# Performance work log

Measured on AMD Instinct MI355X. Metric: run time of the kernel, lower is better.

Reference implementation:

```python
import jax, jax.numpy as jnp
import numpy as np

N_HEAD = 16
SPARSE_TOPK = 64
NEG_INF = float('-inf')


def setup_inputs() -> dict:
    key = jax.random.key(0)
    ks = jax.random.split(key, 12)
    B, T, C = 4, 1024, 1024
    s = 0.02
    q = jax.random.normal(ks[0], (B, T, C), jnp.float32)
    kv = jax.random.normal(ks[1], (B, T, C), jnp.float32)  # forward asserts k == v
    tgt_mask = jnp.tril(jnp.ones((T, T), jnp.bool_)).reshape(1, 1, T, T)
    inp = {'q': q, 'k': kv, 'v': kv, 'tgt_mask': tgt_mask}
    for i, n in enumerate(['Wq', 'Wk', 'Wv', 'Wo']):
        inp[n] = jax.random.normal(ks[2 + i], (C, C), jnp.float32) * s
    for i, n in enumerate(['bq', 'bk', 'bv', 'bo']):
        inp[n] = jax.random.normal(ks[6 + i], (C,), jnp.float32) * s
    return inp


def reference(q, k, v, tgt_mask, Wq, Wk, Wv, Wo, bq, bk, bv, bo):
    B, T, C = q.shape
    H = N_HEAD
    hd = C // H
    scale = 1.0 / np.sqrt(hd).astype(np.float32)
    # QKV projections -> [B, H, T, hd]
    qh = (q @ Wq + bq).reshape(B, T, H, hd).transpose(0, 2, 1, 3)
    kh = (k @ Wk + bk).reshape(B, T, H, hd).transpose(0, 2, 1, 3)
    vh = (v @ Wv + bv).reshape(B, T, H, hd).transpose(0, 2, 1, 3)
    # full attention scores [B, H, T, T]
    att = jnp.einsum('bhtd,bhsd->bhts', qh, kh) * scale
    # causal mask: masked_fill where tgt_mask == 0
    att = jnp.where(tgt_mask[:, :, :T, :T], att, NEG_INF)
    # top-k sparse pruning: keep entries >= k-th largest per row (ties kept)
    top, _ = jax.lax.top_k(att, SPARSE_TOPK)
    vk = top[..., -1:]  # [B, H, T, 1]
    att = jnp.where(att < vk, NEG_INF, att)
    att = jax.nn.softmax(att, axis=-1)
    # dropout is identity in eval (p=0.0)
    y = jnp.einsum('bhts,bhsd->bhtd', att, vh)
    y = y.transpose(0, 2, 1, 3).reshape(B, T, C)
    return y @ Wo + bo
```

## Files before the change

kernel.cpp:

```cpp
#include <hip/hip_runtime.h>
#include <hip/hip_bf16.h>
#include <math.h>

typedef __attribute__((ext_vector_type(8))) short short8;
typedef __attribute__((ext_vector_type(4))) float f32x4;
typedef __attribute__((ext_vector_type(4))) int int4v;

#define SCL 0.1803368801111204f

static __device__ __forceinline__ unsigned short f2bf(float f) {
  unsigned u = __float_as_uint(f);
  u = u + 0x7FFFu + ((u >> 16) & 1u);
  return (unsigned short)(u >> 16);
}

static __device__ __forceinline__ unsigned keyof(float x) {
  unsigned u = __float_as_uint(x);
  return (u & 0x80000000u) ? ~u : (u | 0x80000000u);
}
static __device__ __forceinline__ float keyinv(unsigned k) {
  unsigned u = (k & 0x80000000u) ? (k & 0x7FFFFFFFu) : ~k;
  return __uint_as_float(u);
}

static __device__ __forceinline__ int saddr(int r, int cc) {
  return (((r << 9) + cc) << 2) ^ ((r & 7) << 4);
}
static __device__ __forceinline__ int paddr(int r, int c) {
  return ((r << 11) + (c << 1)) ^ ((r & 7) << 4);
}

static __device__ __forceinline__ void gld_lds16(const unsigned short* g, unsigned short* l) {
  __builtin_amdgcn_global_load_lds(
      (const __attribute__((address_space(1))) void*)g,
      (__attribute__((address_space(3))) void*)l, 16, 0, 0);
}

__global__ __launch_bounds__(256) void cvt3_k(const float* __restrict__ q,
                                              const float* __restrict__ k,
                                              const float* __restrict__ v,
                                              unsigned short* __restrict__ oq,
                                              unsigned short* __restrict__ ok,
                                              unsigned short* __restrict__ ov) {
  const int y = blockIdx.y;
  const float* in = (y == 0) ? q : (y == 1) ? k : v;
  unsigned short* out = (y == 0) ? oq : (y == 1) ? ok : ov;
  const int i = blockIdx.x * 256 + threadIdx.x;
  const f32x4* p = (const f32x4*)in + 2 * (size_t)i;
  f32x4 a = p[0], b = p[1];
  short8 r;
  r[0] = (short)f2bf(a[0]); r[1] = (short)f2bf(a[1]);
  r[2] = (short)f2bf(a[2]); r[3] = (short)f2bf(a[3]);
  r[4] = (short)f2bf(b[0]); r[5] = (short)f2bf(b[1]);
  r[6] = (short)f2bf(b[2]); r[7] = (short)f2bf(b[3]);
  ((short8*)out)[i] = r;
}

__global__ __launch_bounds__(256) void wtrans4_k(const float* __restrict__ Wq,
                                                 const float* __restrict__ Wk,
                                                 const float* __restrict__ Wv,
                                                 const float* __restrict__ Wo,
                                                 unsigned short* __restrict__ Wqt,
                                                 unsigned short* __restrict__ Wkt,
                                                 unsigned short* __restrict__ Wvt,
                                                 unsigned short* __restrict__ Wot) {
  const int z = blockIdx.z;
  const float* W = (z == 0) ? Wq : (z == 1) ? Wk : (z == 2) ? Wv : Wo;
  unsigned short* Wt = (z == 0) ? Wqt : (z == 1) ? Wkt : (z == 2) ? Wvt : Wot;
  __shared__ float tile[32][33];
  const int tx = threadIdx.x, ty = threadIdx.y;
  const int x0 = blockIdx.x * 32, y0 = blockIdx.y * 32;
#pragma unroll
  for (int j = 0; j < 4; ++j)
    tile[ty + j * 8][tx] = W[(y0 + ty + j * 8) * 1024 + x0 + tx];
  __syncthreads();
#pragma unroll
  for (int j = 0; j < 4; ++j)
    Wt[(x0 + ty + j * 8) * 1024 + (y0 + tx)] = f2bf(tile[tx][ty + j * 8]);
}

template <int MODE>
static __device__ __forceinline__ void gemm_body(unsigned short* As, unsigned short* Bs,
                                                 const unsigned short* __restrict__ A,
                                                 const unsigned short* __restrict__ Bt,
                                                 const float* __restrict__ bias,
                                                 void* __restrict__ out) {
  const int tid = threadIdx.x;
  const int lane = tid & 63, w = tid >> 6;
  const int wr = w >> 1, wc = w & 1;
  const int m0 = blockIdx.y * 128, n0 = blockIdx.x * 128;
  const int l15 = lane & 15, l4 = lane >> 4;
  f32x4 acc[4][4] = {};
  const int r0 = tid >> 2, s0 = (tid & 3) * 8;
  const int r1 = r0 + 64;
  const unsigned short* gA0 = A + (m0 + r0) * 1024 + s0;
  const unsigned short* gA1 = A + (m0 + r1) * 1024 + s0;
  const unsigned short* gB0 = Bt + (n0 + r0) * 1024 + s0;
  const unsigned short* gB1 = Bt + (n0 + r1) * 1024 + s0;
  unsigned short* lA0 = As + r0 * 32 + s0;
  unsigned short* lA1 = As + r1 * 32 + s0;
  unsigned short* lB0 = Bs + r0 * 32 + s0;
  unsigned short* lB1 = Bs + r1 * 32 + s0;

  for (int kt = 0; kt < 32; ++kt) {
    const int k0 = kt * 32;
    __syncthreads();
    gld_lds16(gA0 + k0, lA0);
    gld_lds16(gA1 + k0, lA1);
    gld_lds16(gB0 + k0, lB0);
    gld_lds16(gB1 + k0, lB1);
    __syncthreads();
    short8 af[4], bfr[4];
#pragma unroll
    for (int i = 0; i < 4; ++i) {
      af[i]  = *(const short8*)(As + (wr * 64 + i * 16 + l15) * 32 + l4 * 8);
      bfr[i] = *(const short8*)(Bs + (wc * 64 + i * 16 + l15) * 32 + l4 * 8);
    }
#pragma unroll
    for (int i = 0; i < 4; ++i)
#pragma unroll
      for (int j = 0; j < 4; ++j)
        acc[i][j] = __builtin_amdgcn_mfma_f32_16x16x32_bf16(af[i], bfr[j], acc[i][j], 0, 0, 0);
  }
#pragma unroll
  for (int i = 0; i < 4; ++i) {
#pragma unroll
    for (int j = 0; j < 4; ++j) {
      const int n = n0 + wc * 64 + j * 16 + l15;
      const float bv = bias[n];
#pragma unroll
      for (int r = 0; r < 4; ++r) {
        const int m = m0 + wr * 64 + i * 16 + l4 * 4 + r;
        const float v = acc[i][j][r] + bv;
        if (MODE == 2) {
          ((float*)out)[m * 1024 + n] = v;
        } else {
          const int bb = m >> 10, t = m & 1023, hh = n >> 6, dd = n & 63;
          const unsigned short bfv = f2bf(v);
          if (MODE == 0)
            ((unsigned short*)out)[(((bb << 4) + hh) * 1024 + t) * 64 + dd] = bfv;
          else
            ((unsigned short*)out)[(((bb << 4) + hh) * 64 + dd) * 1024 + t] = bfv;
        }
      }
    }
  }
}

__global__ __launch_bounds__(256) void gemm_qkv_k(
    const unsigned short* qbf, const unsigned short* kbf, const unsigned short* vbf,
    const unsigned short* Wqt, const unsigned short* Wkt, const unsigned short* Wvt,
    const float* bq, const float* bk, const float* bv,
    unsigned short* Qh, unsigned short* Kh, unsigned short* Vth) {
  __shared__ unsigned short As[128 * 32], Bs[128 * 32];
  const int z = blockIdx.z;
  const unsigned short* A  = (z == 0) ? qbf : ((z == 1) ? kbf : vbf);
  const unsigned short* Bt = (z == 0) ? Wqt : ((z == 1) ? Wkt : Wvt);
  const float* bias        = (z == 0) ? bq  : ((z == 1) ? bk  : bv);
  if (z == 2) gemm_body<1>(As, Bs, A, Bt, bias, Vth);
  else        gemm_body<0>(As, Bs, A, Bt, bias, z ? Kh : Qh);
}

__global__ __launch_bounds__(256) void gemm_out_k(const unsigned short* Y,
                                                  const unsigned short* Wot,
                                                  const float* bo, float* out) {
  __shared__ unsigned short As[128 * 32], Bs[128 * 32];
  gemm_body<2>(As, Bs, Y, Wot, bo, out);
}

__global__ __launch_bounds__(512, 6) void attn_k(const unsigned short* __restrict__ Q,
                                                 const unsigned short* __restrict__ K,
                                                 const unsigned short* __restrict__ Vt,
                                                 unsigned short* __restrict__ Y) {
  extern __shared__ __align__(16) char smem[];
  const int tid = threadIdx.x, lane = tid & 63, w = tid >> 6;
  const int t0 = (63 - blockIdx.x) * 16;
  const int h = blockIdx.y, b = blockIdx.z;
  const unsigned short* Qp = Q + (((b * 16 + h) * 1024) + t0) * 64;
  const unsigned short* Kh = K + (b * 16 + h) * 65536;
  const unsigned short* Vh = Vt + (b * 16 + h) * 65536;
  const int L = t0 + 16;
  const int Lpad = (L + 31) & ~31;
  const int nCT = L >> 4;
  const int l15 = lane & 15, l4 = lane >> 4;
  float* RED  = (float*)(smem + 32768);
  float* RED2 = (float*)(smem + 32768 + 4352);

  const short8 aq0 = *(const short8*)(Qp + l15 * 64 + l4 * 8);
  const short8 aq1 = *(const short8*)(Qp + l15 * 64 + 32 + l4 * 8);

  auto qk_chunk = [&](int tlo, int thi) {
    for (int ct = tlo + w; ct < thi; ct += 8) {
      const int c0 = ct * 16;
      const short8 kb0 = *(const short8*)(Kh + (c0 + l15) * 64 + l4 * 8);
      const short8 kb1 = *(const short8*)(Kh + (c0 + l15) * 64 + 32 + l4 * 8);
      f32x4 acc = {0.f, 0.f, 0.f, 0.f};
      acc = __builtin_amdgcn_mfma_f32_16x16x32_bf16(aq0, kb0, acc, 0, 0, 0);
      acc = __builtin_amdgcn_mfma_f32_16x16x32_bf16(aq1, kb1, acc, 0, 0, 0);
      const int c = c0 + l15, cc = c & 511;
      if (ct == nCT - 1) {
#pragma unroll
        for (int r = 0; r < 4; ++r) {
          const int row = l4 * 4 + r;
          *(float*)(smem + saddr(row, cc)) = (c <= t0 + row) ? acc[r] * SCL : -INFINITY;
        }
      } else {
#pragma unroll
        for (int r = 0; r < 4; ++r)
          *(float*)(smem + saddr(l4 * 4 + r, cc)) = acc[r] * SCL;
      }
    }
  };

  auto process_row = [&](float (&v)[16], int r, int Lr) {
    float lm = v[0];
#pragma unroll
    for (int i = 1; i < 16; ++i) lm = fmaxf(lm, v[i]);
    float mx = lm, mn = lm;
#pragma unroll
    for (int o = 32; o; o >>= 1) {
      mx = fmaxf(mx, __shfl_xor(mx, o));
      mn = fminf(mn, __shfl_xor(mn, o));
    }
    float thr = -INFINITY;
    if (Lr > 64) {
      unsigned lo = (unsigned)__builtin_amdgcn_readfirstlane((int)keyof(mn));
      unsigned hi = (unsigned)__builtin_amdgcn_readfirstlane((int)keyof(mx)) + 1u;
      int cl = Lr, ch = 0;
      int alt = 0;
      while (hi - lo > 1u) {
        const unsigned span = hi - lo;
        unsigned off;
        if (alt) off = span >> 1;
        else {
          const float fr = (float)(cl - 64) / (float)(cl - ch);
          off = (unsigned)(fr * (float)span);
          if (off < 1u) off = 1u;
          if (off > span - 1u) off = span - 1u;
        }
        alt ^= 1;
        const unsigned mid = lo + off;
        const float tm = keyinv(mid);
        int cnt = 0;
#pragma unroll
        for (int i = 0; i < 16; ++i) cnt += (int)__popcll(__ballot(v[i] >= tm));
        if (cnt >= 64) { lo = mid; cl = cnt; if (cnt == 64) break; }
        else { hi = mid; ch = cnt; }
      }
      thr = keyinv(lo);
    }
    float s = 0.f;
#pragma unroll
    for (int i = 0; i < 16; ++i) {
      const float pv = (v[i] >= thr) ? exp2f(v[i] - mx) : 0.f;
      v[i] = pv;
      s += pv;
    }
#pragma unroll
    for (int o = 32; o; o >>= 1) s += __shfl_xor(s, o);
    if (lane == 0) RED2[r] = 1.f / s;
#pragma unroll
    for (int p = 0; p < 8; ++p) {
      const int c = ((p & 3) << 7) + (lane << 1) + ((p >= 4) ? 512 : 0);
      if (c < Lpad) {
        const unsigned pk = (unsigned)f2bf(v[2 * p]) | ((unsigned)f2bf(v[2 * p + 1]) << 16);
        *(unsigned*)(smem + paddr(r, c)) = pk;
      }
    }
  };

  qk_chunk(0, (nCT < 32) ? nCT : 32);
  __syncthreads();

  const int rA = w * 2, rB = rA + 1;
  const int LrA = t0 + rA + 1, LrB = t0 + rB + 1;
  float vA[16], vB[16];
#pragma unroll
  for (int p = 0; p < 4; ++p) {
    const int c = (p << 7) + (lane << 1);
    const float2 tA = *(const float2*)(smem + saddr(rA, c));
    const float2 tB = *(const float2*)(smem + saddr(rB, c));
    const bool vld = c < L;
    vA[2 * p]     = vld ? tA.x : -INFINITY;
    vA[2 * p + 1] = vld ? tA.y : -INFINITY;
    vB[2 * p]     = vld ? tB.x : -INFINITY;
    vB[2 * p + 1] = vld ? tB.y : -INFINITY;
  }
  __syncthreads();
  if (L > 512) qk_chunk(32, nCT);
  __syncthreads();

#pragma unroll
  for (int p = 0; p < 4; ++p) {
    const int cc = (p << 7) + (lane << 1);
    const float2 tA = *(const float2*)(smem + saddr(rA, cc));
    const bool vld = (cc + 512) < L;
    vA[8 + 2 * p] = vld ? tA.x : -INFINITY;
    vA[9 + 2 * p] = vld ? tA.y : -INFINITY;
  }
  process_row(vA, rA, LrA);

#pragma unroll
  for (int p = 0; p < 4; ++p) {
    const int cc = (p << 7) + (lane << 1);
    const float2 tB = *(const float2*)(smem + saddr(rB, cc));
    const bool vld = (cc + 512) < L;
    vB[8 + 2 * p] = vld ? tB.x : -INFINITY;
    vB[9 + 2 * p] = vld ? tB.y : -INFINITY;
  }
  process_row(vB, rB, LrB);
  __syncthreads();

  const int nST = Lpad >> 5;
  const int stMid = (nST + 1) >> 1;
  const int d0 = (w & 3) * 16;
  const int stLo = (w < 4) ? 0 : stMid;
  const int stHi = (w < 4) ? stMid : nST;
  f32x4 acc = {0.f, 0.f, 0.f, 0.f};
  for (int st = stLo; st < stHi; ++st) {
    const int sb = st * 32 + l4 * 8;
    const short8 paf = *(const short8*)(smem + paddr(l15, sb));
    const short8 vb = *(const short8*)(Vh + (d0 + l15) * 1024 + sb);
    acc = __builtin_amdgcn_mfma_f32_16x16x32_bf16(paf, vb, acc, 0, 0, 0);
  }
  if (w >= 4) {
    const int base = (w - 4) * 272 + l15;
#pragma unroll
    for (int r = 0; r < 4; ++r) RED[base + (l4 * 4 + r) * 17] = acc[r];
  }
  __syncthreads();
  if (w < 4) {
    const int base = w * 272 + l15;
    const int d = (h << 6) + d0 + l15;
#pragma unroll
    for (int r = 0; r < 4; ++r) {
      const float inv = RED2[l4 * 4 + r];
      const float vr = (acc[r] + RED[base + (l4 * 4 + r) * 17]) * inv;
      const int tg = t0 + l4 * 4 + r;
      Y[((b << 10) + tg) * 1024 + d] = f2bf(vr);
    }
  }
}

extern "C" void kernel_launch(void* const* d_in, const int* in_sizes, int n_in,
                              void* d_out, int out_size, void* d_ws, size_t ws_size,
                              hipStream_t stream) {
  const float* q  = (const float*)d_in[0];
  const float* k  = (const float*)d_in[1];
  const float* v  = (const float*)d_in[2];
  const float* Wq = (const float*)d_in[4];
  const float* Wk = (const float*)d_in[5];
  const float* Wv = (const float*)d_in[6];
  const float* Wo = (const float*)d_in[7];
  const float* bq = (const float*)d_in[8];
  const float* bk = (const float*)d_in[9];
  const float* bv = (const float*)d_in[10];
  const float* bo = (const float*)d_in[11];

  char* ws = (char*)d_ws;
  const size_t MB = 1u << 20;
  unsigned short* qbf = (unsigned short*)(ws + 0 * MB);
  unsigned short* kbf = (unsigned short*)(ws + 8 * MB);
  unsigned short* vbf = (unsigned short*)(ws + 16 * MB);
  unsigned short* Wqt = (unsigned short*)(ws + 24 * MB);
  unsigned short* Wkt = (unsigned short*)(ws + 26 * MB);
  unsigned short* Wvt = (unsigned short*)(ws + 28 * MB);
  unsigned short* Wot = (unsigned short*)(ws + 30 * MB);
  unsigned short* Qh  = (unsigned short*)(ws + 32 * MB);
  unsigned short* Kh  = (unsigned short*)(ws + 40 * MB);
  unsigned short* Vth = (unsigned short*)(ws + 48 * MB);
  unsigned short* Y   = qbf;

  cvt3_k<<<dim3(2048, 3), 256, 0, stream>>>(q, k, v, qbf, kbf, vbf);
  wtrans4_k<<<dim3(32, 32, 4), dim3(32, 8), 0, stream>>>(Wq, Wk, Wv, Wo, Wqt, Wkt, Wvt, Wot);
  gemm_qkv_k<<<dim3(8, 32, 3), 256, 0, stream>>>(qbf, kbf, vbf, Wqt, Wkt, Wvt,
                                                 bq, bk, bv, Qh, Kh, Vth);
  attn_k<<<dim3(64, 16, 4), 512, 37248, stream>>>(Qh, Kh, Vth, Y);
  gemm_out_k<<<dim3(8, 32), 256, 0, stream>>>(Y, Wot, bo, (float*)d_out);
}
```

Measured before the change: 230.6 us.

## Halve attention LDS footprint by chunking scores and P into 256/512-column slices

The score buffer now holds 256 columns instead of 512, so QK^T is computed in four column chunks, each followed by a register gather. The bf16 P matrix is kept packed in registers and written to LDS in two 512-column halves, each consumed by its own PV MFMA pass. Shared memory per block drops from about 37KB to about 21KB, which should allow more resident blocks per CU. The cost is extra __syncthreads barriers and more live registers for the packed P values.

```diff
diff --git a/kernel.cpp b/kernel.cpp
--- a/kernel.cpp
+++ b/kernel.cpp
@@ -24,10 +24,10 @@
 }
 
 static __device__ __forceinline__ int saddr(int r, int cc) {
-  return (((r << 9) + cc) << 2) ^ ((r & 7) << 4);
-}
-static __device__ __forceinline__ int paddr(int r, int c) {
-  return ((r << 11) + (c << 1)) ^ ((r & 7) << 4);
+  return (((r << 8) + cc) << 2) ^ ((r & 7) << 4);
+}
+static __device__ __forceinline__ int paddr(int r, int lc) {
+  return ((r << 10) + (lc << 1)) ^ ((r & 7) << 4);
 }
 
 static __device__ __forceinline__ void gld_lds16(const unsigned short* g, unsigned short* l) {
@@ -183,8 +183,8 @@
   const int Lpad = (L + 31) & ~31;
   const int nCT = L >> 4;
   const int l15 = lane & 15, l4 = lane >> 4;
-  float* RED  = (float*)(smem + 32768);
-  float* RED2 = (float*)(smem + 32768 + 4352);
+  float* RED  = (float*)(smem + 16384);
+  float* RED2 = (float*)(smem + 16384 + 4352);
 
   const short8 aq0 = *(const short8*)(Qp + l15 * 64 + l4 * 8);
   const short8 aq1 = *(const short8*)(Qp + l15 * 64 + 32 + l4 * 8);
@@ -197,7 +197,7 @@
       f32x4 acc = {0.f, 0.f, 0.f, 0.f};
       acc = __builtin_amdgcn_mfma_f32_16x16x32_bf16(aq0, kb0, acc, 0, 0, 0);
       acc = __builtin_amdgcn_mfma_f32_16x16x32_bf16(aq1, kb1, acc, 0, 0, 0);
-      const int c = c0 + l15, cc = c & 511;
+      const int c = c0 + l15, cc = c & 255;
       if (ct == nCT - 1) {
 #pragma unroll
         for (int r = 0; r < 4; ++r) {
@@ -212,7 +212,7 @@
     }
   };
 
-  auto process_row = [&](float (&v)[16], int r, int Lr) {
+  auto process_row = [&](float (&v)[16], unsigned (&pk)[8], int r, int Lr) {
     float lm = v[0];
 #pragma unroll
     for (int i = 1; i < 16; ++i) lm = fmaxf(lm, v[i]);
@@ -260,69 +260,96 @@
     for (int o = 32; o; o >>= 1) s += __shfl_xor(s, o);
     if (lane == 0) RED2[r] = 1.f / s;
 #pragma unroll
-    for (int p = 0; p < 8; ++p) {
-      const int c = ((p & 3) << 7) + (lane << 1) + ((p >= 4) ? 512 : 0);
+    for (int p = 0; p < 8; ++p)
+      pk[p] = (unsigned)f2bf(v[2 * p]) | ((unsigned)f2bf(v[2 * p + 1]) << 16);
+  };
+
+  auto write_P = [&](unsigned (&pk)[8], int r, int p) {
+#pragma unroll
+    for (int jj = 0; jj < 4; ++jj) {
+      const int j = 4 * p + jj;
+      const int c = j * 128 + (lane << 1);
       if (c < Lpad) {
-        const unsigned pk = (unsigned)f2bf(v[2 * p]) | ((unsigned)f2bf(v[2 * p + 1]) << 16);
-        *(unsigned*)(smem + paddr(r, c)) = pk;
+        const int lc = c - 512 * p;
+        *(unsigned*)(smem + paddr(r, lc)) = pk[j];
       }
     }
   };
-
-  qk_chunk(0, (nCT < 32) ? nCT : 32);
-  __syncthreads();
 
   const int rA = w * 2, rB = rA + 1;
   const int LrA = t0 + rA + 1, LrB = t0 + rB + 1;
   float vA[16], vB[16];
 #pragma unroll
-  for (int p = 0; p < 4; ++p) {
-    const int c = (p << 7) + (lane << 1);
-    const float2 tA = *(const float2*)(smem + saddr(rA, c));
-    const float2 tB = *(const float2*)(smem + saddr(rB, c));
-    const bool vld = c < L;
-    vA[2 * p]     = vld ? tA.x : -INFINITY;
-    vA[2 * p + 1] = vld ? tA.y : -INFINITY;
-    vB[2 * p]     = vld ? tB.x : -INFINITY;
-    vB[2 * p + 1] = vld ? tB.y : -INFINITY;
-  }
+  for (int c4 = 0; c4 < 4; ++c4) {
+    const int cbase = c4 * 256;
+    if (cbase < L) {
+      const int tlo = c4 * 16;
+      const int thi = (nCT < tlo + 16) ? nCT : (tlo + 16);
+      qk_chunk(tlo, thi);
+      __syncthreads();
+#pragma unroll
+      for (int jj = 0; jj < 2; ++jj) {
+        const int j = 2 * c4 + jj;
+        const int c = j * 128 + (lane << 1);
+        const int cc = c & 255;
+        const float2 tA = *(const float2*)(smem + saddr(rA, cc));
+        const float2 tB = *(const float2*)(smem + saddr(rB, cc));
+        const bool vld = c < L;
+        vA[2 * j]     = vld ? tA.x : -INFINITY;
+        vA[2 * j + 1] = vld ? tA.y : -INFINITY;
+        vB[2 * j]     = vld ? tB.x : -INFINITY;
+        vB[2 * j + 1] = vld ? tB.y : -INFINITY;
+      }
+      __syncthreads();
+    } else {
+#pragma unroll
+      for (int jj = 0; jj < 4; ++jj) {
+        vA[4 * c4 + jj] = -INFINITY;
+        vB[4 * c4 + jj] = -INFINITY;
+      }
+    }
+  }
+
+  unsigned pkA[8], pkB[8];
+  process_row(vA, pkA, rA, LrA);
+  process_row(vB, pkB, rB, LrB);
+
+  const int nSTall = Lpad >> 5;
+  const int nST0 = (nSTall < 16) ? nSTall : 16;
+  const int d0 = (w & 3) * 16;
+  f32x4 acc = {0.f, 0.f, 0.f, 0.f};
+
+  write_P(pkA, rA, 0);
+  write_P(pkB, rB, 0);
   __syncthreads();
-  if (L > 512) qk_chunk(32, nCT);
-  __syncthreads();
-
-#pragma unroll
-  for (int p = 0; p < 4; ++p) {
-    const int cc = (p << 7) + (lane << 1);
-    const float2 tA = *(const float2*)(smem + saddr(rA, cc));
-    const bool vld = (cc + 512) < L;
-    vA[8 + 2 * p] = vld ? tA.x : -INFINITY;
-    vA[9 + 2 * p] = vld ? tA.y : -INFINITY;
-  }
-  process_row(vA, rA, LrA);
-
-#pragma unroll
-  for (int p = 0; p < 4; ++p) {
-    const int cc = (p << 7) + (lane << 1);
-    const float2 tB = *(const float2*)(smem + saddr(rB, cc));
-    const bool vld = (cc + 512) < L;
-    vB[8 + 2 * p] = vld ? tB.x : -INFINITY;
-    vB[9 + 2 * p] = vld ? tB.y : -INFINITY;
-  }
-  process_row(vB, rB, LrB);
-  __syncthreads();
-
-  const int nST = Lpad >> 5;
-  const int stMid = (nST + 1) >> 1;
-  const int d0 = (w & 3) * 16;
-  const int stLo = (w < 4) ? 0 : stMid;
-  const int stHi = (w < 4) ? stMid : nST;
-  f32x4 acc = {0.f, 0.f, 0.f, 0.f};
-  for (int st = stLo; st < stHi; ++st) {
-    const int sb = st * 32 + l4 * 8;
-    const short8 paf = *(const short8*)(smem + paddr(l15, sb));
-    const short8 vb = *(const short8*)(Vh + (d0 + l15) * 1024 + sb);
-    acc = __builtin_amdgcn_mfma_f32_16x16x32_bf16(paf, vb, acc, 0, 0, 0);
-  }
+  {
+    const int stMid = (nST0 + 1) >> 1;
+    const int stLo = (w < 4) ? 0 : stMid;
+    const int stHi = (w < 4) ? stMid : nST0;
+    for (int st = stLo; st < stHi; ++st) {
+      const int sb = st * 32 + l4 * 8;
+      const short8 paf = *(const short8*)(smem + paddr(l15, sb));
+      const short8 vb = *(const short8*)(Vh + (d0 + l15) * 1024 + sb);
+      acc = __builtin_amdgcn_mfma_f32_16x16x32_bf16(paf, vb, acc, 0, 0, 0);
+    }
+  }
+  if (Lpad > 512) {
+    __syncthreads();
+    write_P(pkA, rA, 1);
+    write_P(pkB, rB, 1);
+    __syncthreads();
+    const int nST1 = nSTall - 16;
+    const int stMid = (nST1 + 1) >> 1;
+    const int stLo = (w < 4) ? 0 : stMid;
+    const int stHi = (w < 4) ? stMid : nST1;
+    for (int st = stLo; st < stHi; ++st) {
+      const int sb = st * 32 + l4 * 8;
+      const short8 paf = *(const short8*)(smem + paddr(l15, sb));
+      const short8 vb = *(const short8*)(Vh + (d0 + l15) * 1024 + 512 + sb);
+      acc = __builtin_amdgcn_mfma_f32_16x16x32_bf16(paf, vb, acc, 0, 0, 0);
+    }
+  }
+
   if (w >= 4) {
     const int base = (w - 4) * 272 + l15;
 #pragma unroll
@@ -375,6 +402,6 @@
   wtrans4_k<<<dim3(32, 32, 4), dim3(32, 8), 0, stream>>>(Wq, Wk, Wv, Wo, Wqt, Wkt, Wvt, Wot);
   gemm_qkv_k<<<dim3(8, 32, 3), 256, 0, stream>>>(qbf, kbf, vbf, Wqt, Wkt, Wvt,
                                                  bq, bk, bv, Qh, Kh, Vth);
-  attn_k<<<dim3(64, 16, 4), 512, 37248, stream>>>(Qh, Kh, Vth, Y);
+  attn_k<<<dim3(64, 16, 4), 512, 20800, stream>>>(Qh, Kh, Vth, Y);
   gemm_out_k<<<dim3(8, 32), 256, 0, stream>>>(Y, Wot, bo, (float*)d_out);
 }
```

New measurement: 234.3 us. No clear change (+1.6%).

## Double-buffer GEMM LDS tiles and specialize attention by row length

Applied to the files above, without the earlier changes.

The GEMM main loop now uses two LDS buffers, so the next K-tile's global-to-LDS load is issued before computing on the current tile. This replaces two barriers per iteration with one and lets load latency overlap the MFMAs. The attention kernel is templated on the per-lane value count, giving short rows (t0<512) an 8-value path that skips the second QK chunk, an extra barrier pair and half the top-k counting. The min reduction is now computed only when the top-k search runs. LDS use in the GEMM kernels doubles, which may reduce occupancy.

```diff
diff --git a/kernel.cpp b/kernel.cpp
--- a/kernel.cpp
+++ b/kernel.cpp
@@ -80,7 +80,8 @@
 }
 
 template <int MODE>
-static __device__ __forceinline__ void gemm_body(unsigned short* As, unsigned short* Bs,
+static __device__ __forceinline__ void gemm_body(unsigned short* As0, unsigned short* Bs0,
+                                                 unsigned short* As1, unsigned short* Bs1,
                                                  const unsigned short* __restrict__ A,
                                                  const unsigned short* __restrict__ Bt,
                                                  const float* __restrict__ bias,
@@ -97,30 +98,38 @@
   const unsigned short* gA1 = A + (m0 + r1) * 1024 + s0;
   const unsigned short* gB0 = Bt + (n0 + r0) * 1024 + s0;
   const unsigned short* gB1 = Bt + (n0 + r1) * 1024 + s0;
-  unsigned short* lA0 = As + r0 * 32 + s0;
-  unsigned short* lA1 = As + r1 * 32 + s0;
-  unsigned short* lB0 = Bs + r0 * 32 + s0;
-  unsigned short* lB1 = Bs + r1 * 32 + s0;
+  const int oA0 = r0 * 32 + s0, oA1 = r1 * 32 + s0;
+
+  gld_lds16(gA0, As0 + oA0);
+  gld_lds16(gA1, As0 + oA1);
+  gld_lds16(gB0, Bs0 + oA0);
+  gld_lds16(gB1, Bs0 + oA1);
+  __syncthreads();
 
   for (int kt = 0; kt < 32; ++kt) {
-    const int k0 = kt * 32;
-    __syncthreads();
-    gld_lds16(gA0 + k0, lA0);
-    gld_lds16(gA1 + k0, lA1);
-    gld_lds16(gB0 + k0, lB0);
-    gld_lds16(gB1 + k0, lB1);
-    __syncthreads();
+    if (kt < 31) {
+      const int k0n = (kt + 1) * 32;
+      unsigned short* Asn = (kt & 1) ? As0 : As1;
+      unsigned short* Bsn = (kt & 1) ? Bs0 : Bs1;
+      gld_lds16(gA0 + k0n, Asn + oA0);
+      gld_lds16(gA1 + k0n, Asn + oA1);
+      gld_lds16(gB0 + k0n, Bsn + oA0);
+      gld_lds16(gB1 + k0n, Bsn + oA1);
+    }
+    const unsigned short* Asc = (kt & 1) ? As1 : As0;
+    const unsigned short* Bsc = (kt & 1) ? Bs1 : Bs0;
     short8 af[4], bfr[4];
 #pragma unroll
     for (int i = 0; i < 4; ++i) {
-      af[i]  = *(const short8*)(As + (wr * 64 + i * 16 + l15) * 32 + l4 * 8);
-      bfr[i] = *(const short8*)(Bs + (wc * 64 + i * 16 + l15) * 32 + l4 * 8);
+      af[i]  = *(const short8*)(Asc + (wr * 64 + i * 16 + l15) * 32 + l4 * 8);
+      bfr[i] = *(const short8*)(Bsc + (wc * 64 + i * 16 + l15) * 32 + l4 * 8);
     }
 #pragma unroll
     for (int i = 0; i < 4; ++i)
 #pragma unroll
       for (int j = 0; j < 4; ++j)
         acc[i][j] = __builtin_amdgcn_mfma_f32_16x16x32_bf16(af[i], bfr[j], acc[i][j], 0, 0, 0);
+    __syncthreads();
   }
 #pragma unroll
   for (int i = 0; i < 4; ++i) {
@@ -152,33 +161,90 @@
     const unsigned short* Wqt, const unsigned short* Wkt, const unsigned short* Wvt,
     const float* bq, const float* bk, const float* bv,
     unsigned short* Qh, unsigned short* Kh, unsigned short* Vth) {
-  __shared__ unsigned short As[128 * 32], Bs[128 * 32];
+  __shared__ unsigned short As0[128 * 32], Bs0[128 * 32], As1[128 * 32], Bs1[128 * 32];
   const int z = blockIdx.z;
   const unsigned short* A  = (z == 0) ? qbf : ((z == 1) ? kbf : vbf);
   const unsigned short* Bt = (z == 0) ? Wqt : ((z == 1) ? Wkt : Wvt);
   const float* bias        = (z == 0) ? bq  : ((z == 1) ? bk  : bv);
-  if (z == 2) gemm_body<1>(As, Bs, A, Bt, bias, Vth);
-  else        gemm_body<0>(As, Bs, A, Bt, bias, z ? Kh : Qh);
+  if (z == 2) gemm_body<1>(As0, Bs0, As1, Bs1, A, Bt, bias, Vth);
+  else        gemm_body<0>(As0, Bs0, As1, Bs1, A, Bt, bias, z ? Kh : Qh);
 }
 
 __global__ __launch_bounds__(256) void gemm_out_k(const unsigned short* Y,
                                                   const unsigned short* Wot,
                                                   const float* bo, float* out) {
-  __shared__ unsigned short As[128 * 32], Bs[128 * 32];
-  gemm_body<2>(As, Bs, Y, Wot, bo, out);
-}
-
-__global__ __launch_bounds__(512, 6) void attn_k(const unsigned short* __restrict__ Q,
-                                                 const unsigned short* __restrict__ K,
-                                                 const unsigned short* __restrict__ Vt,
-                                                 unsigned short* __restrict__ Y) {
-  extern __shared__ __align__(16) char smem[];
-  const int tid = threadIdx.x, lane = tid & 63, w = tid >> 6;
-  const int t0 = (63 - blockIdx.x) * 16;
-  const int h = blockIdx.y, b = blockIdx.z;
-  const unsigned short* Qp = Q + (((b * 16 + h) * 1024) + t0) * 64;
-  const unsigned short* Kh = K + (b * 16 + h) * 65536;
-  const unsigned short* Vh = Vt + (b * 16 + h) * 65536;
+  __shared__ unsigned short As0[128 * 32], Bs0[128 * 32], As1[128 * 32], Bs1[128 * 32];
+  gemm_body<2>(As0, Bs0, As1, Bs1, Y, Wot, bo, out);
+}
+
+template <int NVAL>
+static __device__ __forceinline__ void process_row(char* __restrict__ smem, float (&v)[NVAL],
+                                                   const int r, const int Lr, const int Lpad,
+                                                   const int lane, float* __restrict__ RED2) {
+  float lm = v[0];
+#pragma unroll
+  for (int i = 1; i < NVAL; ++i) lm = fmaxf(lm, v[i]);
+  float mx = lm;
+#pragma unroll
+  for (int o = 32; o; o >>= 1) mx = fmaxf(mx, __shfl_xor(mx, o));
+
+  float thr = -INFINITY;
+  if (Lr > 64) {
+    float mn = lm;
+#pragma unroll
+    for (int o = 32; o; o >>= 1) mn = fminf(mn, __shfl_xor(mn, o));
+    unsigned lo = (unsigned)__builtin_amdgcn_readfirstlane((int)keyof(mn));
+    unsigned hi = (unsigned)__builtin_amdgcn_readfirstlane((int)keyof(mx)) + 1u;
+    int cl = Lr, ch = 0, alt = 0;
+    while (hi - lo > 1u) {
+      const unsigned span = hi - lo;
+      unsigned off;
+      if (alt) off = span >> 1;
+      else {
+        const float fr = (float)(cl - 64) / (float)(cl - ch);
+        off = (unsigned)(fr * (float)span);
+        if (off < 1u) off = 1u;
+        if (off > span - 1u) off = span - 1u;
+      }
+      alt ^= 1;
+      const unsigned mid = lo + off;
+      const float tm = keyinv(mid);
+      int cnt = 0;
+#pragma unroll
+      for (int i = 0; i < NVAL; ++i) cnt += (int)__popcll(__ballot(v[i] >= tm));
+      if (cnt >= 64) { lo = mid; cl = cnt; if (cnt == 64) break; }
+      else { hi = mid; ch = cnt; }
+    }
+    thr = keyinv(lo);
+  }
+
+  float s = 0.f;
+  unsigned pk[NVAL / 2];
+#pragma unroll
+  for (int p = 0; p < NVAL / 2; ++p) {
+    const float p0 = (v[2 * p]     >= thr) ? exp2f(v[2 * p]     - mx) : 0.f;
+    const float p1 = (v[2 * p + 1] >= thr) ? exp2f(v[2 * p + 1] - mx) : 0.f;
+    s += p0 + p1;
+    pk[p] = (unsigned)f2bf(p0) | ((unsigned)f2bf(p1) << 16);
+  }
+#pragma unroll
+  for (int o = 32; o; o >>= 1) s += __shfl_xor(s, o);
+  if (lane == 0) RED2[r] = 1.f / s;
+#pragma unroll
+  for (int p = 0; p < NVAL / 2; ++p) {
+    const int c = ((p & 3) << 7) + (lane << 1) + ((p >= 4) ? 512 : 0);
+    if (c < Lpad) *(unsigned*)(smem + paddr(r, c)) = pk[p];
+  }
+}
+
+template <int NVAL>
+static __device__ __forceinline__ void attn_body(char* __restrict__ smem,
+                                                 const unsigned short* __restrict__ Qp,
+                                                 const unsigned short* __restrict__ Kh,
+                                                 const unsigned short* __restrict__ Vh,
+                                                 unsigned short* __restrict__ Y,
+                                                 const int t0, const int h, const int b,
+                                                 const int lane, const int w) {
   const int L = t0 + 16;
   const int Lpad = (L + 31) & ~31;
   const int nCT = L >> 4;
@@ -212,69 +278,12 @@
     }
   };
 
-  auto process_row = [&](float (&v)[16], int r, int Lr) {
-    float lm = v[0];
-#pragma unroll
-    for (int i = 1; i < 16; ++i) lm = fmaxf(lm, v[i]);
-    float mx = lm, mn = lm;
-#pragma unroll
-    for (int o = 32; o; o >>= 1) {
-      mx = fmaxf(mx, __shfl_xor(mx, o));
-      mn = fminf(mn, __shfl_xor(mn, o));
-    }
-    float thr = -INFINITY;
-    if (Lr > 64) {
-      unsigned lo = (unsigned)__builtin_amdgcn_readfirstlane((int)keyof(mn));
-      unsigned hi = (unsigned)__builtin_amdgcn_readfirstlane((int)keyof(mx)) + 1u;
-      int cl = Lr, ch = 0;
-      int alt = 0;
-      while (hi - lo > 1u) {
-        const unsigned span = hi - lo;
-        unsigned off;
-        if (alt) off = span >> 1;
-        else {
-          const float fr = (float)(cl - 64) / (float)(cl - ch);
-          off = (unsigned)(fr * (float)span);
-          if (off < 1u) off = 1u;
-          if (off > span - 1u) off = span - 1u;
-        }
-        alt ^= 1;
-        const unsigned mid = lo + off;
-        const float tm = keyinv(mid);
-        int cnt = 0;
-#pragma unroll
-        for (int i = 0; i < 16; ++i) cnt += (int)__popcll(__ballot(v[i] >= tm));
-        if (cnt >= 64) { lo = mid; cl = cnt; if (cnt == 64) break; }
-        else { hi = mid; ch = cnt; }
-      }
-      thr = keyinv(lo);
-    }
-    float s = 0.f;
-#pragma unroll
-    for (int i = 0; i < 16; ++i) {
-      const float pv = (v[i] >= thr) ? exp2f(v[i] - mx) : 0.f;
-      v[i] = pv;
-      s += pv;
-    }
-#pragma unroll
-    for (int o = 32; o; o >>= 1) s += __shfl_xor(s, o);
-    if (lane == 0) RED2[r] = 1.f / s;
-#pragma unroll
-    for (int p = 0; p < 8; ++p) {
-      const int c = ((p & 3) << 7) + (lane << 1) + ((p >= 4) ? 512 : 0);
-      if (c < Lpad) {
-        const unsigned pk = (unsigned)f2bf(v[2 * p]) | ((unsigned)f2bf(v[2 * p + 1]) << 16);
-        *(unsigned*)(smem + paddr(r, c)) = pk;
-      }
-    }
-  };
-
   qk_chunk(0, (nCT < 32) ? nCT : 32);
   __syncthreads();
 
   const int rA = w * 2, rB = rA + 1;
   const int LrA = t0 + rA + 1, LrB = t0 + rB + 1;
-  float vA[16], vB[16];
+  float vA[NVAL], vB[NVAL];
 #pragma unroll
   for (int p = 0; p < 4; ++p) {
     const int c = (p << 7) + (lane << 1);
@@ -286,29 +295,33 @@
     vB[2 * p]     = vld ? tB.x : -INFINITY;
     vB[2 * p + 1] = vld ? tB.y : -INFINITY;
   }
-  __syncthreads();
-  if (L > 512) qk_chunk(32, nCT);
-  __syncthreads();
-
-#pragma unroll
-  for (int p = 0; p < 4; ++p) {
-    const int cc = (p << 7) + (lane << 1);
-    const float2 tA = *(const float2*)(smem + saddr(rA, cc));
-    const bool vld = (cc + 512) < L;
-    vA[8 + 2 * p] = vld ? tA.x : -INFINITY;
-    vA[9 + 2 * p] = vld ? tA.y : -INFINITY;
-  }
-  process_row(vA, rA, LrA);
-
-#pragma unroll
-  for (int p = 0; p < 4; ++p) {
-    const int cc = (p << 7) + (lane << 1);
-    const float2 tB = *(const float2*)(smem + saddr(rB, cc));
-    const bool vld = (cc + 512) < L;
-    vB[8 + 2 * p] = vld ? tB.x : -INFINITY;
-    vB[9 + 2 * p] = vld ? tB.y : -INFINITY;
-  }
-  process_row(vB, rB, LrB);
+
+  if constexpr (NVAL == 16) {
+    __syncthreads();
+    qk_chunk(32, nCT);
+    __syncthreads();
+#pragma unroll
+    for (int p = 0; p < 4; ++p) {
+      const int cc = (p << 7) + (lane << 1);
+      const float2 tA = *(const float2*)(smem + saddr(rA, cc));
+      const bool vld = (cc + 512) < L;
+      vA[8 + 2 * p] = vld ? tA.x : -INFINITY;
+      vA[9 + 2 * p] = vld ? tA.y : -INFINITY;
+    }
+    process_row<NVAL>(smem, vA, rA, LrA, Lpad, lane, RED2);
+#pragma unroll
+    for (int p = 0; p < 4; ++p) {
+      const int cc = (p << 7) + (lane << 1);
+      const float2 tB = *(const float2*)(smem + saddr(rB, cc));
+      const bool vld = (cc + 512) < L;
+      vB[8 + 2 * p] = vld ? tB.x : -INFINITY;
+      vB[9 + 2 * p] = vld ? tB.y : -INFINITY;
+    }
+    process_row<NVAL>(smem, vB, rB, LrB, Lpad, lane, RED2);
+  } else {
+    process_row<NVAL>(smem, vA, rA, LrA, Lpad, lane, RED2);
+    process_row<NVAL>(smem, vB, rB, LrB, Lpad, lane, RED2);
+  }
   __syncthreads();
 
   const int nST = Lpad >> 5;
@@ -340,6 +353,21 @@
       Y[((b << 10) + tg) * 1024 + d] = f2bf(vr);
     }
   }
+}
+
+__global__ __launch_bounds__(512, 6) void attn_k(const unsigned short* __restrict__ Q,
+                                                 const unsigned short* __restrict__ K,
+                                                 const unsigned short* __restrict__ Vt,
+                                                 unsigned short* __restrict__ Y) {
+  extern __shared__ __align__(16) char smem[];
+  const int tid = threadIdx.x, lane = tid & 63, w = tid >> 6;
+  const int t0 = (63 - (int)blockIdx.x) * 16;
+  const int h = blockIdx.y, b = blockIdx.z;
+  const unsigned short* Qp = Q + (((b * 16 + h) * 1024) + t0) * 64;
+  const unsigned short* Kh = K + (b * 16 + h) * 65536;
+  const unsigned short* Vh = Vt + (b * 16 + h) * 65536;
+  if (t0 >= 512) attn_body<16>(smem, Qp, Kh, Vh, Y, t0, h, b, lane, w);
+  else           attn_body<8>(smem, Qp, Kh, Vh, Y, t0, h, b, lane, w);
 }
 
 extern "C" void kernel_launch(void* const* d_in, const int* in_sizes, int n_in,
```

New measurement: 211.3 us. -8.4%, faster.
